# Kernel tuning notes

Hardware: AMD Instinct MI355X
Metric: run time of the kernel (lower is better)

The kernel has to match this reference:

```python
import jax, jax.numpy as jnp
import numpy as np
from jax import lax

ITERATIONS = 8
KT, KH, KW = 3, 7, 7


def _ssm_op(left, right):
    a1, b1 = left
    a2, b2 = right
    return (a1 * a2, a2 * b1 + b2)


def setup_inputs() -> dict:
    key = jax.random.key(0)
    k1, k2, k3 = jax.random.split(key, 3)
    B, T, H, W, C = 1, 16, 64, 64, 128
    x = jax.random.normal(k1, (B, T, H, W, C), dtype=jnp.float32)
    A_kernel = 0.02 * jax.random.normal(k2, (C, KT, KH, KW), dtype=jnp.float32)
    B_kernel = 0.02 * jax.random.normal(k3, (C, KT, KH, KW), dtype=jnp.float32)
    return {"x": x, "A_kernel": A_kernel, "B_kernel": B_kernel}


def _pad_kernel_fft(kern, T, H, W):
    # Place (C, kt, kh, kw) kernel circularly centered into a (C, T, H, W) canvas, FFT it.
    C = kern.shape[0]
    t_idx = (jnp.arange(KT) - KT // 2) % T
    h_idx = (jnp.arange(KH) - KH // 2) % H
    w_idx = (jnp.arange(KW) - KW // 2) % W
    tt, th, tw = jnp.meshgrid(t_idx, h_idx, w_idx, indexing="ij")
    padded = jnp.zeros((C, T, H, W), dtype=kern.dtype).at[:, tt, th, tw].set(kern)
    kf = jnp.fft.fftn(padded, axes=(1, 2, 3))  # (C, T, H, W) complex
    return kf.transpose(1, 2, 3, 0)[None, ...]  # (1, T, H, W, C)


def reference(x, A_kernel, B_kernel):
    B, T, H, W, C = x.shape
    A_stable = 0.9 * jnp.tanh(A_kernel)
    A_f = _pad_kernel_fft(A_stable, T, H, W)   # (1,T,H,W,C)
    B_f = _pad_kernel_fft(B_kernel, T, H, W)   # (1,T,H,W,C)
    x_f = jnp.fft.fftn(x, axes=(1, 2, 3))      # (B,T,H,W,C)
    Bx_f = B_f * x_f
    a_seq = jnp.broadcast_to(A_f, (ITERATIONS, B, T, H, W, C))
    b_seq = jnp.broadcast_to(Bx_f, (ITERATIONS, B, T, H, W, C))
    _, h_all_f = lax.associative_scan(_ssm_op, (a_seq, b_seq), axis=0)
    h_final = jnp.fft.ifftn(h_all_f[-1], axes=(1, 2, 3)).real
    return h_final
```

## Files before the change

kernel.cpp:

```cpp
#include <hip/hip_runtime.h>
#include <hip/hip_fp16.h>
#include <math.h>

#define TT 16
#define HH 64
#define WW 64
#define CC 128

#define LROW(r) (((r) & 0x38) | ((((r) >> 3) ^ (r)) & 7))

__device__ __forceinline__ float2 cadd(float2 a, float2 b){ return make_float2(a.x+b.x, a.y+b.y); }
__device__ __forceinline__ float2 csub(float2 a, float2 b){ return make_float2(a.x-b.x, a.y-b.y); }
__device__ __forceinline__ float2 cmul(float2 a, float2 b) {
    return make_float2(a.x*b.x - a.y*b.y, a.x*b.y + a.y*b.x);
}
__device__ __forceinline__ float2 cmac(float2 acc, float2 a, float2 b) {
    acc.x = fmaf(a.x, b.x, fmaf(-a.y, b.y, acc.x));
    acc.y = fmaf(a.x, b.y, fmaf(a.y, b.x, acc.y));
    return acc;
}
__device__ __forceinline__ float2 csq(float2 a) {
    return make_float2(a.x*a.x - a.y*a.y, 2.f*a.x*a.y);
}

template<int SGN>
__device__ __forceinline__ void dft4(float2 b0, float2 b1, float2 b2, float2 b3,
                                     float2& y0, float2& y1, float2& y2, float2& y3) {
    float2 e0 = cadd(b0, b2), e1 = csub(b0, b2);
    float2 o0 = cadd(b1, b3), o1 = csub(b1, b3);
    y0 = cadd(e0, o0); y2 = csub(e0, o0);
    float2 r = make_float2((float)(-SGN) * o1.y, (float)SGN * o1.x);
    y1 = cadd(e1, r); y3 = csub(e1, r);
}

template<int SGN>
__device__ __forceinline__ void dft8(const float2* a, float2* X) {
    const float C = 0.70710678118654752f;
    float2 E0,E1,E2,E3,O0,O1,O2,O3;
    dft4<SGN>(a[0],a[2],a[4],a[6], E0,E1,E2,E3);
    dft4<SGN>(a[1],a[3],a[5],a[7], O0,O1,O2,O3);
    float2 T1 = make_float2(C*(O1.x - (float)SGN*O1.y), C*((float)SGN*O1.x + O1.y));
    float2 T2 = make_float2((float)(-SGN)*O2.y, (float)SGN*O2.x);
    float2 T3 = make_float2(-C*(O3.x + (float)SGN*O3.y), C*((float)SGN*O3.x - O3.y));
    X[0]=cadd(E0,O0); X[4]=csub(E0,O0);
    X[1]=cadd(E1,T1); X[5]=csub(E1,T1);
    X[2]=cadd(E2,T2); X[6]=csub(E2,T2);
    X[3]=cadd(E3,T3); X[7]=csub(E3,T3);
}

template<int SGN>
__device__ __forceinline__ void dft16(const float2* v, float2* X) {
    const float ct[10] = {1.f, 0.92387953251f, 0.70710678119f, 0.38268343236f, 0.f,
                          0.f, -0.70710678119f, 0.f, 0.f, -0.92387953251f};
    const float st[10] = {0.f, 0.38268343236f, 0.70710678119f, 0.92387953251f, 1.f,
                          0.f, 0.70710678119f, 0.f, 0.f, -0.38268343236f};
    float2 Z[16];
    #pragma unroll
    for (int h0 = 0; h0 < 4; ++h0) {
        float2 y0,y1,y2,y3;
        dft4<SGN>(v[h0], v[4+h0], v[8+h0], v[12+h0], y0,y1,y2,y3);
        float2 ys[4] = {y0,y1,y2,y3};
        #pragma unroll
        for (int k0 = 0; k0 < 4; ++k0) {
            int m = h0 * k0;
            float cc = ct[m], ss = (float)SGN * st[m];
            Z[k0*4 + h0] = make_float2(ys[k0].x*cc - ys[k0].y*ss,
                                       ys[k0].x*ss + ys[k0].y*cc);
        }
    }
    #pragma unroll
    for (int k0 = 0; k0 < 4; ++k0) {
        float2 y0,y1,y2,y3;
        dft4<SGN>(Z[k0*4+0], Z[k0*4+1], Z[k0*4+2], Z[k0*4+3], y0,y1,y2,y3);
        X[k0] = y0; X[k0+4] = y1; X[k0+8] = y2; X[k0+12] = y3;
    }
}

__global__ __launch_bounds__(256) void k_prep(const float* __restrict__ Ak,
                                              const float* __restrict__ Bk,
                                              __half2* __restrict__ Ahw,
                                              __half2* __restrict__ Bhw) {
    __shared__ float Asl[7][7][64];
    __shared__ float Bsl[7][7][64];
    __shared__ float2 Awl[7][64];
    __shared__ float2 Bwl[7][64];
    __shared__ float2 tw64[64];
    int bid = blockIdx.x;
    int kt = bid / 66;
    int rem = bid % 66;
    int om = rem >> 1, chalf = rem & 1;
    int c0 = chalf * 64;
    int tid = threadIdx.x;
    for (int i = tid; i < 64; i += 256) {
        float s, cq; sincosf(-6.283185307179586f * i / 64.0f, &s, &cq);
        tw64[i] = make_float2(cq, s);
    }
    for (int i = tid; i < 49 * 64; i += 256) {
        int p = i >> 6, cl = i & 63;
        int kh = p / 7, kw = p % 7;
        int idx = (((c0 + cl) * 3 + kt) * 7 + kh) * 7 + kw;
        Asl[kh][kw][cl] = 0.9f * tanhf(Ak[idx]);
        Bsl[kh][kw][cl] = Bk[idx];
    }
    __syncthreads();
    for (int i = tid; i < 7 * 64; i += 256) {
        int kh = i >> 6, cl = i & 63;
        float2 aA = make_float2(0.f,0.f), aB = make_float2(0.f,0.f);
        #pragma unroll
        for (int kw = 0; kw < 7; ++kw) {
            float2 t = tw64[(om * (kw - 3)) & 63];
            float va = Asl[kh][kw][cl], vb = Bsl[kh][kw][cl];
            aA.x = fmaf(va, t.x, aA.x); aA.y = fmaf(va, t.y, aA.y);
            aB.x = fmaf(vb, t.x, aB.x); aB.y = fmaf(vb, t.y, aB.y);
        }
        Awl[kh][cl] = aA; Bwl[kh][cl] = aB;
    }
    __syncthreads();
    for (int i = tid; i < 64 * 64; i += 256) {
        int eta = i >> 6, cl = i & 63;
        float2 aA = make_float2(0.f,0.f), aB = make_float2(0.f,0.f);
        #pragma unroll
        for (int kh = 0; kh < 7; ++kh) {
            float2 t = tw64[(eta * (kh - 3)) & 63];
            aA = cmac(aA, Awl[kh][cl], t);
            aB = cmac(aB, Bwl[kh][cl], t);
        }
        int ep = ((eta & 7) << 3) | (eta >> 3);
        int o = ((kt * 33 + om) * 64 + ep) * 128 + c0 + cl;
        Ahw[o] = __float22half2_rn(aA);
        Bhw[o] = __float22half2_rn(aB);
    }
}


__global__ __launch_bounds__(512) void p1(const float* __restrict__ x,
                                          uint4* __restrict__ Z) {
    __shared__ float rf[64][64];
    __shared__ __half2 sp[4][33][64];
    __shared__ float2 tw64[64];
    __half2* zal = (__half2*)&rf[0][0];
    int bid = blockIdx.x;
    int t = bid >> 5, hq = (bid >> 1) & 15, chalf = bid & 1;
    int tid = threadIdx.x;
    if (tid < 64) {
        float s, cq; sincosf(-6.283185307179586f * tid / 64.0f, &s, &cq);
        tw64[tid] = make_float2(cq, s);
    }
    int c = tid & 63, s4 = tid >> 6;
    for (int hh = 0; hh < 4; ++hh) {
        const float4* src4 = (const float4*)(x + (size_t)(t*64 + hq*4 + hh) * 64 * 128
                                               + chalf * 64);
        for (int i = tid; i < 1024; i += 512) {
            int w = i >> 4, c4 = (i & 15) * 4;
            float4 v = src4[w * 32 + (i & 15)];
            rf[w][c4] = v.x; rf[w][c4+1] = v.y; rf[w][c4+2] = v.z; rf[w][c4+3] = v.w;
        }
        __syncthreads();
        float ar[8];
        #pragma unroll
        for (int h1 = 0; h1 < 8; ++h1) ar[h1] = rf[h1*8 + s4][c];
        __syncthreads();
        {
            float2 a[8], Y[8];
            #pragma unroll
            for (int h1 = 0; h1 < 8; ++h1) a[h1] = make_float2(ar[h1], 0.f);
            dft8<-1>(a, Y);
            #pragma unroll
            for (int k0 = 0; k0 < 8; ++k0) {
                float2 z = cmul(Y[k0], tw64[(s4 * k0) & 63]);
                zal[(k0*8 + s4) * 64 + c] = __float22half2_rn(z);
            }
        }
        __syncthreads();
        {
            float2 b[8], X[8];
            #pragma unroll
            for (int h0 = 0; h0 < 8; ++h0)
                b[h0] = __half22float2(zal[(s4*8 + h0) * 64 + c]);
            dft8<-1>(b, X);
            #pragma unroll
            for (int k1 = 0; k1 < 8; ++k1) {
                int om = s4 + 8 * k1;
                if (om <= 32) sp[hh][om][c] = __float22half2_rn(X[k1]);
            }
        }
        __syncthreads();
    }
    for (int i = tid; i < 2112; i += 512) {
        int hh = i & 3, ccl = (i >> 2) & 15, om = i >> 6;
        int cb = ccl * 4;
        uint4 u;
        __half2 v0 = sp[hh][om][cb+0], v1 = sp[hh][om][cb+1];
        __half2 v2 = sp[hh][om][cb+2], v3 = sp[hh][om][cb+3];
        u.x = *(unsigned int*)&v0; u.y = *(unsigned int*)&v1;
        u.z = *(unsigned int*)&v2; u.w = *(unsigned int*)&v3;
        Z[(((size_t)(om*32 + chalf*16 + ccl)*16 + t)*64 + hq*4 + hh)] = u;
    }
}

__global__ __launch_bounds__(256) void pmid(uint4* __restrict__ Z,
                                            const __half2* __restrict__ Ahw,
                                            const __half2* __restrict__ Bhw) {
    __shared__ __half2 tl[16][64][4];
    int l = (blockIdx.x & 7) * 132 + (blockIdx.x >> 3);
    int om = l >> 5, cc = l & 31;
    int c0 = cc * 4;
    int tid = threadIdx.x;
    uint4* g = Z + (size_t)l * 1024;

    int d = tid & 7;
    float twc[8], tws[8];
    {
        float s1, c1; sincosf(-6.283185307179586f * d / 64.0f, &s1, &c1);
        twc[0] = 1.f; tws[0] = 0.f;
        #pragma unroll
        for (int k = 1; k < 8; ++k) {
            twc[k] = twc[k-1]*c1 - tws[k-1]*s1;
            tws[k] = twc[k-1]*s1 + tws[k-1]*c1;
        }
    }
    for (int i = tid; i < 1024; i += 256) {
        uint4 u = g[i];
        int t = i >> 6, h = i & 63;
        int pr = LROW(h);
        tl[t][pr][0] = *(__half2*)&u.x;
        tl[t][pr][1] = *(__half2*)&u.y;
        tl[t][pr][2] = *(__half2*)&u.z;
        tl[t][pr][3] = *(__half2*)&u.w;
    }
    __syncthreads();
    int cl = (tid >> 3) & 3, ts = tid >> 5;
    #pragma unroll
    for (int q = 0; q < 2; ++q) {
        int t = ts*2 + q;
        float2 a[8], Y[8];
        #pragma unroll
        for (int h1 = 0; h1 < 8; ++h1)
            a[h1] = __half22float2(tl[t][LROW(h1*8 + d)][cl]);
        dft8<-1>(a, Y);
        #pragma unroll
        for (int k0 = 0; k0 < 8; ++k0) {
            float2 z = make_float2(Y[k0].x*twc[k0] - Y[k0].y*tws[k0],
                                   Y[k0].x*tws[k0] + Y[k0].y*twc[k0]);
            tl[t][LROW(k0*8 + d)][cl] = __float22half2_rn(z);
        }
    }
    __syncthreads();
    #pragma unroll
    for (int q = 0; q < 2; ++q) {
        int t = ts*2 + q;
        float2 a[8], Y[8];
        #pragma unroll
        for (int h0 = 0; h0 < 8; ++h0)
            a[h0] = __half22float2(tl[t][LROW(d*8 + h0)][cl]);
        dft8<-1>(a, Y);
        #pragma unroll
        for (int k1 = 0; k1 < 8; ++k1)
            tl[t][LROW(d*8 + k1)][cl] = __float22half2_rn(Y[k1]);
    }
    __syncthreads();
    {
        const float CT16[16] = {1.f, 0.9238795325f, 0.7071067812f, 0.3826834324f, 0.f,
                                -0.3826834324f, -0.7071067812f, -0.9238795325f, -1.f,
                                -0.9238795325f, -0.7071067812f, -0.3826834324f, 0.f,
                                0.3826834324f, 0.7071067812f, 0.9238795325f};
        const float ST16[16] = {0.f, 0.3826834324f, 0.7071067812f, 0.9238795325f, 1.f,
                                0.9238795325f, 0.7071067812f, 0.3826834324f, 0.f,
                                -0.3826834324f, -0.7071067812f, -0.9238795325f, -1.f,
                                -0.9238795325f, -0.7071067812f, -0.3826834324f};
        int cg = tid & 3, rT = tid >> 2;
        const int PKT = 33 * 64 * 128;
        int kb = (om * 64 + rT) * 128 + c0 + cg;
        float2 A0 = __half22float2(Ahw[kb]);
        float2 A1 = __half22float2(Ahw[kb + PKT]);
        float2 A2 = __half22float2(Ahw[kb + 2*PKT]);
        float2 B0 = __half22float2(Bhw[kb]);
        float2 B1 = __half22float2(Bhw[kb + PKT]);
        float2 B2 = __half22float2(Bhw[kb + 2*PKT]);
        int pr = LROW(rT);
        float2 v[16], X[16];
        #pragma unroll
        for (int t = 0; t < 16; ++t) v[t] = __half22float2(tl[t][pr][cg]);
        dft16<-1>(v, X);
        #pragma unroll
        for (int ta = 0; ta < 16; ++ta) {
            float2 wv = make_float2(CT16[ta], -ST16[ta]);
            float2 wc = make_float2(CT16[ta],  ST16[ta]);
            float2 Af = A1; Af = cmac(Af, A0, wc); Af = cmac(Af, A2, wv);
            float2 Bf = B1; Bf = cmac(Bf, B0, wc); Bf = cmac(Bf, B2, wv);
            float2 A2q = csq(Af), A4q = csq(A2q);
            float2 S = cmul(make_float2(1.f+Af.x, Af.y), make_float2(1.f+A2q.x, A2q.y));
            S = cmul(S, make_float2(1.f+A4q.x, A4q.y));
            float2 G = cmul(S, Bf);
            X[ta] = cmul(X[ta], G);
        }
        dft16<1>(X, v);
        const float sc = 0.015625f;
        #pragma unroll
        for (int t = 0; t < 16; ++t)
            tl[t][pr][cg] = __float22half2_rn(make_float2(v[t].x*sc, v[t].y*sc));
    }
    __syncthreads();
    #pragma unroll
    for (int q = 0; q < 2; ++q) {
        int t = ts*2 + q;
        float2 a[8], Y[8];
        #pragma unroll
        for (int e1 = 0; e1 < 8; ++e1)
            a[e1] = __half22float2(tl[t][LROW(d*8 + e1)][cl]);
        dft8<1>(a, Y);
        #pragma unroll
        for (int h0 = 0; h0 < 8; ++h0) {
            float2 z = make_float2( Y[h0].x*twc[h0] + Y[h0].y*tws[h0],
                                   -Y[h0].x*tws[h0] + Y[h0].y*twc[h0]);
            tl[t][LROW(d*8 + h0)][cl] = __float22half2_rn(z);
        }
    }
    __syncthreads();
    #pragma unroll
    for (int q = 0; q < 2; ++q) {
        int t = ts*2 + q;
        float2 a[8], Y[8];
        #pragma unroll
        for (int e0 = 0; e0 < 8; ++e0)
            a[e0] = __half22float2(tl[t][LROW(e0*8 + d)][cl]);
        dft8<1>(a, Y);
        #pragma unroll
        for (int h1 = 0; h1 < 8; ++h1)
            tl[t][LROW(d + 8*h1)][cl] = __float22half2_rn(Y[h1]);
    }
    __syncthreads();
    for (int i = tid; i < 1024; i += 256) {
        int t = i >> 6, h = i & 63;
        int pr = LROW(h);
        uint4 u;
        __half2 v0 = tl[t][pr][0], v1 = tl[t][pr][1];
        __half2 v2 = tl[t][pr][2], v3 = tl[t][pr][3];
        u.x = *(unsigned int*)&v0; u.y = *(unsigned int*)&v1;
        u.z = *(unsigned int*)&v2; u.w = *(unsigned int*)&v3;
        g[i] = u;
    }
}

__global__ __launch_bounds__(512) void p5(const uint4* __restrict__ Z,
                                          float* __restrict__ out) {
    __shared__ __half2 sp[4][33][64];
    __shared__ __half2 plane[64][64];
    __shared__ float2 tw64[64];
    int bid = blockIdx.x;
    int t = bid >> 5, hq = (bid >> 1) & 15, chalf = bid & 1;
    int tid = threadIdx.x;
    if (tid < 64) {
        float s, cq; sincosf(6.283185307179586f * tid / 64.0f, &s, &cq);
        tw64[tid] = make_float2(cq, s);
    }
    for (int i = tid; i < 2112; i += 512) {
        int hh = i & 3, ccl = (i >> 2) & 15, om = i >> 6;
        uint4 u = Z[(((size_t)(om*32 + chalf*16 + ccl)*16 + t)*64 + hq*4 + hh)];
        int cb = ccl * 4;
        sp[hh][om][cb+0] = *(__half2*)&u.x;
        sp[hh][om][cb+1] = *(__half2*)&u.y;
        sp[hh][om][cb+2] = *(__half2*)&u.z;
        sp[hh][om][cb+3] = *(__half2*)&u.w;
    }
    __syncthreads();
    int c = tid & 63, s4 = tid >> 6;
    for (int hh = 0; hh < 4; ++hh) {
        for (int i = tid; i < 33 * 64; i += 512) {
            int om = i >> 6, cl = i & 63;
            __half2 v = sp[hh][om][cl];
            plane[om][cl] = v;
            if (om >= 1 && om <= 31) {
                __half2 m = v; m.y = __hneg(m.y);
                plane[64 - om][cl] = m;
            }
        }
        __syncthreads();
        float2 ar[8];
        #pragma unroll
        for (int h1 = 0; h1 < 8; ++h1)
            ar[h1] = __half22float2(plane[h1*8 + s4][c]);
        __syncthreads();
        {
            float2 Y[8];
            dft8<1>(ar, Y);
            #pragma unroll
            for (int k0 = 0; k0 < 8; ++k0) {
                float2 z = cmul(Y[k0], tw64[(s4 * k0) & 63]);
                plane[k0*8 + s4][c] = __float22half2_rn(z);
            }
        }
        __syncthreads();
        {
            float2 b[8], X[8];
            #pragma unroll
            for (int h0 = 0; h0 < 8; ++h0)
                b[h0] = __half22float2(plane[s4*8 + h0][c]);
            dft8<1>(b, X);
            float* dst = out + (size_t)(t*64 + hq*4 + hh) * 64 * 128 + chalf * 64 + c;
            #pragma unroll
            for (int k1 = 0; k1 < 8; ++k1)
                dst[(size_t)(s4 + 8*k1) * 128] = X[k1].x * (1.0f / 1024.0f);
        }
        __syncthreads();
    }
}

extern "C" void kernel_launch(void* const* d_in, const int* in_sizes, int n_in,
                              void* d_out, int out_size, void* d_ws, size_t ws_size,
                              hipStream_t stream) {
    const float* x  = (const float*)d_in[0];
    const float* Ak = (const float*)d_in[1];
    const float* Bk = (const float*)d_in[2];
    float* out = (float*)d_out;

    uint4* Z = (uint4*)d_ws;
    __half2* Ahw = (__half2*)((char*)d_ws + (size_t)33*32*1024*16);
    __half2* Bhw = Ahw + 3 * 33 * 64 * 128;

    hipLaunchKernelGGL(k_prep, dim3(198),  dim3(256), 0, stream, Ak, Bk, Ahw, Bhw);
    hipLaunchKernelGGL(p1,     dim3(512),  dim3(512), 0, stream, x, Z);
    hipLaunchKernelGGL(pmid,   dim3(1056), dim3(256), 0, stream, Z, Ahw, Bhw);
    hipLaunchKernelGGL(p5,     dim3(512),  dim3(512), 0, stream, Z, out);
}
```

Before: 68.66 us.

## Merge kernel prep into first FFT pass and split channels into quarters

Fuses the kernel-spectrum preparation and the first (H,W) FFT pass into one launch, using block-index branching over a shared smem buffer, which removes one kernel launch and lets the two independent jobs overlap. Both the forward and the inverse plane-FFT kernels now process 32 channels per block with 256 threads instead of 64 channels with 512 threads, doubling the block count for better occupancy and load balance. The cost is less coalesced global access per block (128-byte channel segments) and a heterogeneous grid in which the prep blocks run a different workload.

After: 65.76 us. 4.2% less time.

```diff
diff --git a/kernel.cpp b/kernel.cpp
--- a/kernel.cpp
+++ b/kernel.cpp
@@ -6,6 +6,7 @@
 #define HH 64
 #define WW 64
 #define CC 128
+#define PI2 6.283185307179586f
 
 #define LROW(r) (((r) & 0x38) | ((((r) >> 3) ^ (r)) & 7))
 
@@ -76,125 +77,121 @@
     }
 }
 
-__global__ __launch_bounds__(256) void k_prep(const float* __restrict__ Ak,
-                                              const float* __restrict__ Bk,
-                                              __half2* __restrict__ Ahw,
-                                              __half2* __restrict__ Bhw) {
-    __shared__ float Asl[7][7][64];
-    __shared__ float Bsl[7][7][64];
-    __shared__ float2 Awl[7][64];
-    __shared__ float2 Bwl[7][64];
-    __shared__ float2 tw64[64];
+
+__global__ __launch_bounds__(256) void pA(const float* __restrict__ x,
+                                          uint4* __restrict__ Z,
+                                          const float* __restrict__ Ak,
+                                          const float* __restrict__ Bk,
+                                          __half2* __restrict__ Ahw,
+                                          __half2* __restrict__ Bhw) {
+    __shared__ __align__(16) char smem[33280];
     int bid = blockIdx.x;
-    int kt = bid / 66;
-    int rem = bid % 66;
-    int om = rem >> 1, chalf = rem & 1;
-    int c0 = chalf * 64;
     int tid = threadIdx.x;
-    for (int i = tid; i < 64; i += 256) {
-        float s, cq; sincosf(-6.283185307179586f * i / 64.0f, &s, &cq);
-        tw64[i] = make_float2(cq, s);
-    }
-    for (int i = tid; i < 49 * 64; i += 256) {
-        int p = i >> 6, cl = i & 63;
-        int kh = p / 7, kw = p % 7;
-        int idx = (((c0 + cl) * 3 + kt) * 7 + kh) * 7 + kw;
-        Asl[kh][kw][cl] = 0.9f * tanhf(Ak[idx]);
-        Bsl[kh][kw][cl] = Bk[idx];
-    }
-    __syncthreads();
-    for (int i = tid; i < 7 * 64; i += 256) {
-        int kh = i >> 6, cl = i & 63;
-        float2 aA = make_float2(0.f,0.f), aB = make_float2(0.f,0.f);
-        #pragma unroll
-        for (int kw = 0; kw < 7; ++kw) {
-            float2 t = tw64[(om * (kw - 3)) & 63];
-            float va = Asl[kh][kw][cl], vb = Bsl[kh][kw][cl];
-            aA.x = fmaf(va, t.x, aA.x); aA.y = fmaf(va, t.y, aA.y);
-            aB.x = fmaf(vb, t.x, aB.x); aB.y = fmaf(vb, t.y, aB.y);
-        }
-        Awl[kh][cl] = aA; Bwl[kh][cl] = aB;
-    }
-    __syncthreads();
-    for (int i = tid; i < 64 * 64; i += 256) {
-        int eta = i >> 6, cl = i & 63;
-        float2 aA = make_float2(0.f,0.f), aB = make_float2(0.f,0.f);
-        #pragma unroll
-        for (int kh = 0; kh < 7; ++kh) {
-            float2 t = tw64[(eta * (kh - 3)) & 63];
-            aA = cmac(aA, Awl[kh][cl], t);
-            aB = cmac(aB, Bwl[kh][cl], t);
-        }
-        int ep = ((eta & 7) << 3) | (eta >> 3);
-        int o = ((kt * 33 + om) * 64 + ep) * 128 + c0 + cl;
-        Ahw[o] = __float22half2_rn(aA);
-        Bhw[o] = __float22half2_rn(aB);
-    }
-}
-
-
-__global__ __launch_bounds__(512) void p1(const float* __restrict__ x,
-                                          uint4* __restrict__ Z) {
-    __shared__ float rf[64][64];
-    __shared__ __half2 sp[4][33][64];
-    __shared__ float2 tw64[64];
-    __half2* zal = (__half2*)&rf[0][0];
-    int bid = blockIdx.x;
-    int t = bid >> 5, hq = (bid >> 1) & 15, chalf = bid & 1;
-    int tid = threadIdx.x;
-    if (tid < 64) {
-        float s, cq; sincosf(-6.283185307179586f * tid / 64.0f, &s, &cq);
-        tw64[tid] = make_float2(cq, s);
-    }
-    int c = tid & 63, s4 = tid >> 6;
-    for (int hh = 0; hh < 4; ++hh) {
-        const float4* src4 = (const float4*)(x + (size_t)(t*64 + hq*4 + hh) * 64 * 128
-                                               + chalf * 64);
-        for (int i = tid; i < 1024; i += 512) {
-            int w = i >> 4, c4 = (i & 15) * 4;
-            float4 v = src4[w * 32 + (i & 15)];
-            rf[w][c4] = v.x; rf[w][c4+1] = v.y; rf[w][c4+2] = v.z; rf[w][c4+3] = v.w;
-        }
-        __syncthreads();
-        float ar[8];
-        #pragma unroll
-        for (int h1 = 0; h1 < 8; ++h1) ar[h1] = rf[h1*8 + s4][c];
-        __syncthreads();
-        {
-            float2 a[8], Y[8];
-            #pragma unroll
-            for (int h1 = 0; h1 < 8; ++h1) a[h1] = make_float2(ar[h1], 0.f);
-            dft8<-1>(a, Y);
-            #pragma unroll
-            for (int k0 = 0; k0 < 8; ++k0) {
-                float2 z = cmul(Y[k0], tw64[(s4 * k0) & 63]);
-                zal[(k0*8 + s4) * 64 + c] = __float22half2_rn(z);
-            }
-        }
-        __syncthreads();
-        {
-            float2 b[8], X[8];
-            #pragma unroll
-            for (int h0 = 0; h0 < 8; ++h0)
-                b[h0] = __half22float2(zal[(s4*8 + h0) * 64 + c]);
-            dft8<-1>(b, X);
-            #pragma unroll
-            for (int k1 = 0; k1 < 8; ++k1) {
-                int om = s4 + 8 * k1;
-                if (om <= 32) sp[hh][om][c] = __float22half2_rn(X[k1]);
-            }
-        }
-        __syncthreads();
-    }
-    for (int i = tid; i < 2112; i += 512) {
-        int hh = i & 3, ccl = (i >> 2) & 15, om = i >> 6;
-        int cb = ccl * 4;
-        uint4 u;
-        __half2 v0 = sp[hh][om][cb+0], v1 = sp[hh][om][cb+1];
-        __half2 v2 = sp[hh][om][cb+2], v3 = sp[hh][om][cb+3];
-        u.x = *(unsigned int*)&v0; u.y = *(unsigned int*)&v1;
-        u.z = *(unsigned int*)&v2; u.w = *(unsigned int*)&v3;
-        Z[(((size_t)(om*32 + chalf*16 + ccl)*16 + t)*64 + hq*4 + hh)] = u;
+    if (bid < 1024) {
+        float (*rf)[32]        = (float(*)[32])smem;
+        __half2 (*sp)[33][32]  = (__half2(*)[33][32])(smem + 8192);
+        float2* tw64           = (float2*)(smem + 8192 + 16896);
+        __half2* zal           = (__half2*)smem;
+        int cq = bid & 3, hq = (bid >> 2) & 15, t = bid >> 6;
+        if (tid < 64) {
+            float s, cw; sincosf(-PI2 * tid / 64.0f, &s, &cw);
+            tw64[tid] = make_float2(cw, s);
+        }
+        int c = tid & 31, s4 = tid >> 5;
+        for (int hh = 0; hh < 4; ++hh) {
+            const float4* src4 = (const float4*)(x + (size_t)(t*64 + hq*4 + hh) * 64 * 128);
+            for (int i = tid; i < 512; i += 256) {
+                int w = i >> 3, j = i & 7;
+                float4 v = src4[w * 32 + cq * 8 + j];
+                rf[w][j*4+0] = v.x; rf[w][j*4+1] = v.y;
+                rf[w][j*4+2] = v.z; rf[w][j*4+3] = v.w;
+            }
+            __syncthreads();
+            float ar[8];
+            #pragma unroll
+            for (int h1 = 0; h1 < 8; ++h1) ar[h1] = rf[h1*8 + s4][c];
+            __syncthreads();
+            {
+                float2 a[8], Y[8];
+                #pragma unroll
+                for (int h1 = 0; h1 < 8; ++h1) a[h1] = make_float2(ar[h1], 0.f);
+                dft8<-1>(a, Y);
+                #pragma unroll
+                for (int k0 = 0; k0 < 8; ++k0) {
+                    float2 z = cmul(Y[k0], tw64[(s4 * k0) & 63]);
+                    zal[(k0*8 + s4) * 32 + c] = __float22half2_rn(z);
+                }
+            }
+            __syncthreads();
+            {
+                float2 b[8], X[8];
+                #pragma unroll
+                for (int h0 = 0; h0 < 8; ++h0)
+                    b[h0] = __half22float2(zal[(s4*8 + h0) * 32 + c]);
+                dft8<-1>(b, X);
+                #pragma unroll
+                for (int k1 = 0; k1 < 8; ++k1) {
+                    int om = s4 + 8 * k1;
+                    if (om <= 32) sp[hh][om][c] = __float22half2_rn(X[k1]);
+                }
+            }
+            __syncthreads();
+        }
+        for (int i = tid; i < 1056; i += 256) {
+            int hh = i & 3, ccl = (i >> 2) & 7, om = i >> 5;
+            uint4 u = *(const uint4*)&sp[hh][om][ccl * 4];
+            Z[(((size_t)(om*32 + cq*8 + ccl)*16 + t)*64 + hq*4 + hh)] = u;
+        }
+    } else {
+        float (*Asl)[7][64] = (float(*)[7][64])smem;
+        float (*Bsl)[7][64] = (float(*)[7][64])(smem + 12544);
+        float2 (*Awl)[64]   = (float2(*)[64])(smem + 25088);
+        float2 (*Bwl)[64]   = (float2(*)[64])(smem + 28672);
+        float2* tw64        = (float2*)(smem + 32256);
+        int kid = bid - 1024;
+        int kt = kid / 66;
+        int rem = kid % 66;
+        int om = rem >> 1, chalf = rem & 1;
+        int c0 = chalf * 64;
+        for (int i = tid; i < 64; i += 256) {
+            float s, cw; sincosf(-PI2 * i / 64.0f, &s, &cw);
+            tw64[i] = make_float2(cw, s);
+        }
+        for (int i = tid; i < 49 * 64; i += 256) {
+            int p = i >> 6, cl = i & 63;
+            int kh = p / 7, kw = p % 7;
+            int idx = (((c0 + cl) * 3 + kt) * 7 + kh) * 7 + kw;
+            Asl[kh][kw][cl] = 0.9f * tanhf(Ak[idx]);
+            Bsl[kh][kw][cl] = Bk[idx];
+        }
+        __syncthreads();
+        for (int i = tid; i < 7 * 64; i += 256) {
+            int kh = i >> 6, cl = i & 63;
+            float2 aA = make_float2(0.f,0.f), aB = make_float2(0.f,0.f);
+            #pragma unroll
+            for (int kw = 0; kw < 7; ++kw) {
+                float2 tw = tw64[(om * (kw - 3)) & 63];
+                float va = Asl[kh][kw][cl], vb = Bsl[kh][kw][cl];
+                aA.x = fmaf(va, tw.x, aA.x); aA.y = fmaf(va, tw.y, aA.y);
+                aB.x = fmaf(vb, tw.x, aB.x); aB.y = fmaf(vb, tw.y, aB.y);
+            }
+            Awl[kh][cl] = aA; Bwl[kh][cl] = aB;
+        }
+        __syncthreads();
+        for (int i = tid; i < 64 * 64; i += 256) {
+            int eta = i >> 6, cl = i & 63;
+            float2 aA = make_float2(0.f,0.f), aB = make_float2(0.f,0.f);
+            #pragma unroll
+            for (int kh = 0; kh < 7; ++kh) {
+                float2 tw = tw64[(eta * (kh - 3)) & 63];
+                aA = cmac(aA, Awl[kh][cl], tw);
+                aB = cmac(aB, Bwl[kh][cl], tw);
+            }
+            int ep = ((eta & 7) << 3) | (eta >> 3);
+            int o = ((kt * 33 + om) * 64 + ep) * 128 + c0 + cl;
+            Ahw[o] = __float22half2_rn(aA);
+            Bhw[o] = __float22half2_rn(aB);
+        }
     }
 }
 
@@ -211,7 +208,7 @@
     int d = tid & 7;
     float twc[8], tws[8];
     {
-        float s1, c1; sincosf(-6.283185307179586f * d / 64.0f, &s1, &c1);
+        float s1, c1; sincosf(-PI2 * d / 64.0f, &s1, &c1);
         twc[0] = 1.f; tws[0] = 0.f;
         #pragma unroll
         for (int k = 1; k < 8; ++k) {
@@ -342,32 +339,28 @@
     }
 }
 
-__global__ __launch_bounds__(512) void p5(const uint4* __restrict__ Z,
+__global__ __launch_bounds__(256) void p5(const uint4* __restrict__ Z,
                                           float* __restrict__ out) {
-    __shared__ __half2 sp[4][33][64];
-    __shared__ __half2 plane[64][64];
+    __shared__ __half2 sp[4][33][32];
+    __shared__ __half2 plane[64][32];
     __shared__ float2 tw64[64];
     int bid = blockIdx.x;
-    int t = bid >> 5, hq = (bid >> 1) & 15, chalf = bid & 1;
+    int cq = bid & 3, hq = (bid >> 2) & 15, t = bid >> 6;
     int tid = threadIdx.x;
     if (tid < 64) {
-        float s, cq; sincosf(6.283185307179586f * tid / 64.0f, &s, &cq);
-        tw64[tid] = make_float2(cq, s);
-    }
-    for (int i = tid; i < 2112; i += 512) {
-        int hh = i & 3, ccl = (i >> 2) & 15, om = i >> 6;
-        uint4 u = Z[(((size_t)(om*32 + chalf*16 + ccl)*16 + t)*64 + hq*4 + hh)];
-        int cb = ccl * 4;
-        sp[hh][om][cb+0] = *(__half2*)&u.x;
-        sp[hh][om][cb+1] = *(__half2*)&u.y;
-        sp[hh][om][cb+2] = *(__half2*)&u.z;
-        sp[hh][om][cb+3] = *(__half2*)&u.w;
-    }
-    __syncthreads();
-    int c = tid & 63, s4 = tid >> 6;
+        float s, cw; sincosf(PI2 * tid / 64.0f, &s, &cw);
+        tw64[tid] = make_float2(cw, s);
+    }
+    for (int i = tid; i < 1056; i += 256) {
+        int hh = i & 3, ccl = (i >> 2) & 7, om = i >> 5;
+        uint4 u = Z[(((size_t)(om*32 + cq*8 + ccl)*16 + t)*64 + hq*4 + hh)];
+        *(uint4*)&sp[hh][om][ccl * 4] = u;
+    }
+    __syncthreads();
+    int c = tid & 31, s4 = tid >> 5;
     for (int hh = 0; hh < 4; ++hh) {
-        for (int i = tid; i < 33 * 64; i += 512) {
-            int om = i >> 6, cl = i & 63;
+        for (int i = tid; i < 1056; i += 256) {
+            int om = i >> 5, cl = i & 31;
             __half2 v = sp[hh][om][cl];
             plane[om][cl] = v;
             if (om >= 1 && om <= 31) {
@@ -397,7 +390,7 @@
             for (int h0 = 0; h0 < 8; ++h0)
                 b[h0] = __half22float2(plane[s4*8 + h0][c]);
             dft8<1>(b, X);
-            float* dst = out + (size_t)(t*64 + hq*4 + hh) * 64 * 128 + chalf * 64 + c;
+            float* dst = out + (size_t)(t*64 + hq*4 + hh) * 64 * 128 + cq * 32 + c;
             #pragma unroll
             for (int k1 = 0; k1 < 8; ++k1)
                 dst[(size_t)(s4 + 8*k1) * 128] = X[k1].x * (1.0f / 1024.0f);
@@ -418,8 +411,7 @@
     __half2* Ahw = (__half2*)((char*)d_ws + (size_t)33*32*1024*16);
     __half2* Bhw = Ahw + 3 * 33 * 64 * 128;
 
-    hipLaunchKernelGGL(k_prep, dim3(198),  dim3(256), 0, stream, Ak, Bk, Ahw, Bhw);
-    hipLaunchKernelGGL(p1,     dim3(512),  dim3(512), 0, stream, x, Z);
-    hipLaunchKernelGGL(pmid,   dim3(1056), dim3(256), 0, stream, Z, Ahw, Bhw);
-    hipLaunchKernelGGL(p5,     dim3(512),  dim3(512), 0, stream, Z, out);
-}
+    hipLaunchKernelGGL(pA,   dim3(1222), dim3(256), 0, stream, x, Z, Ak, Bk, Ahw, Bhw);
+    hipLaunchKernelGGL(pmid, dim3(1056), dim3(256), 0, stream, Z, Ahw, Bhw);
+    hipLaunchKernelGGL(p5,   dim3(1024), dim3(256), 0, stream, Z, out);
+}
```
